# Kernel optimization log

Hardware: AMD Instinct MI355X
Metric: run time of the kernel (lower is better)

## Reference

```python
import jax, jax.numpy as jnp
import numpy as np

N = 50000      # nodes
HID = 128      # hidden_dim
E = 1600000    # edges per sparse operator (avg degree 32)


def _spmm(rows, cols, vals, x):
    # y = A @ x for COO sparse A: gather source rows, scale, scatter-add to dest rows
    return jax.ops.segment_sum(vals[:, None] * x[cols], rows, num_segments=N)


def setup_inputs() -> dict:
    key = jax.random.key(0)
    ks = jax.random.split(key, 22)

    def edges(i):
        return (jax.random.randint(ks[i], (E,), 0, N, dtype=jnp.int64) if jax.config.jax_enable_x64 else jax.random.randint(ks[i], (E,), 0, N).astype(jnp.int32),
                jax.random.randint(ks[i + 1], (E,), 0, N).astype(jnp.int32),
                jax.random.uniform(ks[i + 2], (E,), jnp.float32))

    A_rows, A_cols, A_vals = edges(0)
    P1_rows, P1_cols, P1_vals = edges(3)
    P2_rows, P2_cols, P2_vals = edges(6)
    P3_rows, P3_cols, P3_vals = edges(9)
    Ps_rows, Ps_cols, Ps_vals = edges(12)

    X = jax.random.normal(ks[15], (N, HID), jnp.float32)
    a = jax.random.normal(ks[16], (2 * HID, 1), jnp.float32) * 0.1
    W1 = jax.random.normal(ks[17], (HID, HID), jnp.float32) / jnp.sqrt(HID)
    b1 = jnp.zeros((HID,), jnp.float32)
    W2 = jax.random.normal(ks[18], (HID, HID), jnp.float32) / jnp.sqrt(HID)
    b2 = jnp.zeros((HID,), jnp.float32)

    return dict(X=X, a=a, W1=W1, b1=b1, W2=W2, b2=b2,
                A_rows=A_rows, A_cols=A_cols, A_vals=A_vals,
                P1_rows=P1_rows, P1_cols=P1_cols, P1_vals=P1_vals,
                P2_rows=P2_rows, P2_cols=P2_cols, P2_vals=P2_vals,
                P3_rows=P3_rows, P3_cols=P3_cols, P3_vals=P3_vals,
                Psct_rows=Ps_rows, Psct_cols=Ps_cols, Psct_vals=Ps_vals)


def reference(X, a, W1, b1, W2, b2,
              A_rows, A_cols, A_vals,
              P1_rows, P1_cols, P1_vals,
              P2_rows, P2_cols, P2_vals,
              P3_rows, P3_cols, P3_vals,
              Psct_rows, Psct_cols, Psct_vals):
    h = X  # [N, HID]
    h_A = _spmm(A_rows, A_cols, A_vals, h)
    h_A2 = _spmm(A_rows, A_cols, A_vals, h_A)
    h_A3 = _spmm(A_rows, A_cols, A_vals, h_A2)
    # moment = 1 => |P x| ** 1
    h_s1 = jnp.abs(_spmm(P1_rows, P1_cols, P1_vals, h))
    h_s2 = jnp.abs(_spmm(P2_rows, P2_cols, P2_vals, h))
    h_s3 = jnp.abs(_spmm(P3_rows, P3_cols, P3_vals, h))

    # Faithful to torch: cat along dim 0 then view(N, -1, 2*hid) (row-interleaved layout)
    def pair(hb):
        return jnp.concatenate([h, hb], axis=0).reshape(N, 1, 2 * HID)

    a_input = jnp.concatenate(
        [pair(h_A), pair(h_A2), pair(h_A3), pair(h_s1), pair(h_s2), pair(h_s3)],
        axis=1)  # [N, 6, 2*HID]

    e = jnp.squeeze(jax.nn.relu(a_input) @ a, axis=2)          # [N, 6]
    attention = jax.nn.softmax(e, axis=1).reshape(N, 6, 1)     # [N, 6, 1]

    # Faithful to torch: cat along dim 2 -> [N, HID, 6], then view(N, 6, -1)
    h_all = jnp.concatenate(
        [h_A[:, :, None], h_A2[:, :, None], h_A3[:, :, None],
         h_s1[:, :, None], h_s2[:, :, None], h_s3[:, :, None]],
        axis=2).reshape(N, 6, HID)

    h_prime = jnp.mean(attention * h_all, axis=1)              # [N, HID]

    # Withgres=False: skip gres smoothing (P_sct unused)
    out = jax.nn.leaky_relu(h_prime @ W1.T + b1)               # slope 0.01, matches torch default
    out = jax.nn.leaky_relu(out @ W2.T + b2)
    return out
```

## Files before the change

kernel.cpp:

```cpp
#include <hip/hip_runtime.h>
#include <hip/hip_fp16.h>

#define N_NODES 50000
#define HID 128
#define NE 1600000
#define NH (N_NODES * HID)

#define EPB   8192
#define NBLK1 196
#define NBUK  391
#define TBL   (NBUK * NBLK1)
#define SB    ((TBL + 255) / 256)
#define PTRW  (N_NODES + 2)

typedef _Float16 f16x8 __attribute__((ext_vector_type(8)));
typedef float    f32x4 __attribute__((ext_vector_type(4)));

__device__ __forceinline__ float h2f(unsigned short u) {
    __half_raw r; r.x = u;
    __half h = r;
    return __half2float(h);
}
__device__ __forceinline__ unsigned short f2h(float f) {
    __half h = __float2half_rn(f);
    __half_raw r = h;
    return r.x;
}

__global__ __launch_bounds__(256) void k1_hist4(
    const int* __restrict__ r0, const int* __restrict__ r1,
    const int* __restrict__ r2, const int* __restrict__ r3,
    int* __restrict__ table4, unsigned short* __restrict__ rank4)
{
    __shared__ int h[NBUK];
    int o = blockIdx.y, b = blockIdx.x, t = threadIdx.x;
    const int* rows = o == 0 ? r0 : o == 1 ? r1 : o == 2 ? r2 : r3;
    int* table = table4 + (size_t)o * TBL;
    unsigned short* rank = rank4 + (size_t)o * NE;

    for (int i = t; i < NBUK; i += 256) h[i] = 0;
    __syncthreads();
    int e0 = b * EPB;
    int e1 = min(e0 + EPB, NE);
    for (int e = e0 + t; e < e1; e += 256)
        rank[e] = (unsigned short)atomicAdd(&h[rows[e] >> 7], 1);
    __syncthreads();
    for (int i = t; i < NBUK; i += 256) table[i * NBLK1 + b] = h[i];
}

__global__ __launch_bounds__(256) void s1_partial4(
    const int* __restrict__ table4, int* __restrict__ part4)
{
    __shared__ int red[256];
    int o = blockIdx.y, b = blockIdx.x, t = threadIdx.x;
    const int* table = table4 + (size_t)o * TBL;
    int idx = b * 256 + t;
    red[t] = (idx < TBL) ? table[idx] : 0;
    __syncthreads();
    #pragma unroll
    for (int s = 128; s > 0; s >>= 1) {
        if (t < s) red[t] += red[t + s];
        __syncthreads();
    }
    if (t == 0) part4[o * SB + b] = red[0];
}

__global__ __launch_bounds__(1024) void s2_scan4(int* __restrict__ part4)
{
    __shared__ int sh[1024];
    int o = blockIdx.x, t = threadIdx.x;
    int* part = part4 + o * SB;
    sh[t] = (t < SB) ? part[t] : 0;
    __syncthreads();
    for (int off = 1; off < 1024; off <<= 1) {
        int v = (t >= off) ? sh[t - off] : 0;
        __syncthreads();
        sh[t] += v;
        __syncthreads();
    }
    if (t < SB) part[t] = (t == 0) ? 0 : sh[t - 1];
}

__global__ __launch_bounds__(256) void s3_add4(
    int* __restrict__ table4, const int* __restrict__ part4)
{
    __shared__ int sh[256];
    int o = blockIdx.y, b = blockIdx.x, t = threadIdx.x;
    int* table = table4 + (size_t)o * TBL;
    int idx = b * 256 + t;
    int v = (idx < TBL) ? table[idx] : 0;
    sh[t] = v;
    __syncthreads();
    #pragma unroll
    for (int off = 1; off < 256; off <<= 1) {
        int u = (t >= off) ? sh[t - off] : 0;
        __syncthreads();
        sh[t] += u;
        __syncthreads();
    }
    int excl = (t == 0) ? 0 : sh[t - 1];
    if (idx < TBL) table[idx] = part4[o * SB + b] + excl;
}

__global__ __launch_bounds__(256) void k3_scatter4(
    const int* __restrict__ r0, const int* __restrict__ r1,
    const int* __restrict__ r2, const int* __restrict__ r3,
    const int* __restrict__ c0, const int* __restrict__ c1,
    const int* __restrict__ c2, const int* __restrict__ c3,
    const float* __restrict__ v0, const float* __restrict__ v1,
    const float* __restrict__ v2, const float* __restrict__ v3,
    const unsigned short* __restrict__ rank4,
    const int* __restrict__ table4, int2* __restrict__ tmp4)
{
    __shared__ int base[NBUK];
    int o = blockIdx.y, b = blockIdx.x, t = threadIdx.x;
    const int*   rows = o == 0 ? r0 : o == 1 ? r1 : o == 2 ? r2 : r3;
    const int*   cols = o == 0 ? c0 : o == 1 ? c1 : o == 2 ? c2 : c3;
    const float* vals = o == 0 ? v0 : o == 1 ? v1 : o == 2 ? v2 : v3;
    const int* table = table4 + (size_t)o * TBL;
    const unsigned short* rank = rank4 + (size_t)o * NE;
    int2* tmp = tmp4 + (size_t)o * NE;

    for (int i = t; i < NBUK; i += 256) base[i] = table[i * NBLK1 + b];
    __syncthreads();
    int e0 = b * EPB;
    int e1 = min(e0 + EPB, NE);
    for (int e = e0 + t; e < e1; e += 256) {
        int r = rows[e];
        int pos = base[r >> 7] + (int)rank[e];
        unsigned pk = ((unsigned)cols[e] << 16) | (unsigned)f2h(vals[e]);
        tmp[pos] = make_int2(r & 127, (int)pk);
    }
}

__global__ __launch_bounds__(256) void k4_fine4(
    const int* __restrict__ table4, const int2* __restrict__ tmp4,
    unsigned* __restrict__ pairs4, int* __restrict__ ptr4)
{
    __shared__ int cnt[128];
    __shared__ int sh[256];
    __shared__ int nxt[128];
    int o = blockIdx.y, k = blockIdx.x, t = threadIdx.x;
    const int* table = table4 + (size_t)o * TBL;
    const int2* tmp = tmp4 + (size_t)o * NE;
    unsigned* pairs = pairs4 + (size_t)o * NE;
    int* rowptr = ptr4 + (size_t)o * PTRW;

    if (t < 128) cnt[t] = 0;
    __syncthreads();
    int base = table[k * NBLK1];
    int end  = (k == NBUK - 1) ? NE : table[(k + 1) * NBLK1];
    for (int e = base + t; e < end; e += 256)
        atomicAdd(&cnt[tmp[e].x], 1);
    __syncthreads();
    sh[t] = (t < 128) ? cnt[t] : 0;
    __syncthreads();
    #pragma unroll
    for (int off = 1; off < 256; off <<= 1) {
        int v = (t >= off) ? sh[t - off] : 0;
        __syncthreads();
        sh[t] += v;
        __syncthreads();
    }
    if (t < 128) {
        int excl = (t == 0) ? 0 : sh[t - 1];
        nxt[t] = base + excl;
        int row = k * 128 + t;
        if (row < N_NODES) rowptr[row] = base + excl;
    }
    if (k == NBUK - 1 && t == 255) rowptr[N_NODES] = NE;
    __syncthreads();
    for (int e = base + t; e < end; e += 256) {
        int2 p = tmp[e];
        int pos = atomicAdd(&nxt[p.x], 1);
        pairs[pos] = (unsigned)p.y;
    }
}

__global__ __launch_bounds__(256) void cvt_f2h_kernel(
    const float* __restrict__ in, unsigned short* __restrict__ out, int n4)
{
    int i = blockIdx.x * 256 + threadIdx.x;
    if (i >= n4) return;
    float4 v = ((const float4*)in)[i];
    ushort4 o;
    o.x = f2h(v.x); o.y = f2h(v.y); o.z = f2h(v.z); o.w = f2h(v.w);
    ((ushort4*)out)[i] = o;
}

__device__ __forceinline__ void spmm_row(
    const unsigned short* __restrict__ xh, const unsigned* __restrict__ pairs,
    int start, int end, int sub, bool do_abs,
    unsigned short* __restrict__ yrow)
{
    const ushort4* x4 = (const ushort4*)xh + sub;

    float4 a0 = {0,0,0,0}, a1 = {0,0,0,0};
    float4 a2 = {0,0,0,0}, a3 = {0,0,0,0};

    #define EDGE_P(P, A) { \
        unsigned _p = (P); \
        float _v = h2f((unsigned short)(_p & 0xFFFFu)); \
        ushort4 _x = x4[(size_t)(_p >> 16) * 32]; \
        A.x += _v * h2f(_x.x); \
        A.y += _v * h2f(_x.y); \
        A.z += _v * h2f(_x.z); \
        A.w += _v * h2f(_x.w); }

    int e = start;
    for (; e + 3 < end; e += 4) {
        unsigned p0 = pairs[e];
        unsigned p1 = pairs[e + 1];
        unsigned p2 = pairs[e + 2];
        unsigned p3 = pairs[e + 3];
        EDGE_P(p0, a0); EDGE_P(p1, a1); EDGE_P(p2, a2); EDGE_P(p3, a3);
    }
    for (; e < end; ++e) {
        EDGE_P(pairs[e], a0);
    }
    #undef EDGE_P

    float4 acc;
    acc.x = (a0.x + a1.x) + (a2.x + a3.x);
    acc.y = (a0.y + a1.y) + (a2.y + a3.y);
    acc.z = (a0.z + a1.z) + (a2.z + a3.z);
    acc.w = (a0.w + a1.w) + (a2.w + a3.w);
    if (do_abs) {
        acc.x = fabsf(acc.x); acc.y = fabsf(acc.y);
        acc.z = fabsf(acc.z); acc.w = fabsf(acc.w);
    }
    ushort4 o;
    o.x = f2h(acc.x); o.y = f2h(acc.y); o.z = f2h(acc.z); o.w = f2h(acc.w);
    ((ushort4*)yrow)[sub] = o;
}

__global__ __launch_bounds__(256) void spmm4_kernel(
    const int* __restrict__ ptr4, const unsigned* __restrict__ pairs4,
    const unsigned short* __restrict__ Xh, unsigned short* __restrict__ B16)
{
    int bid = blockIdx.x;
    int op  = bid & 3;
    int rb  = bid >> 2;
    int r   = rb * 8 + (threadIdx.x >> 5);
    int sub = threadIdx.x & 31;
    if (r >= N_NODES) return;

    const int*      ptr   = ptr4 + (size_t)op * PTRW;
    const unsigned* pairs = pairs4 + (size_t)op * NE;
    int dst = op ? op + 2 : 0;
    unsigned short* yrow = B16 + (size_t)dst * NH + (size_t)r * HID;

    spmm_row(Xh, pairs, ptr[r], ptr[r + 1], sub, op != 0, yrow);
}

__global__ __launch_bounds__(256) void spmm_chain_kernel(
    const int* __restrict__ ptr, const unsigned* __restrict__ pairs,
    const unsigned short* __restrict__ src16, unsigned short* __restrict__ dst16)
{
    int t   = blockIdx.x * 256 + threadIdx.x;
    int r   = t >> 5;
    int sub = t & 31;
    if (r >= N_NODES) return;
    spmm_row(src16, pairs, ptr[r], ptr[r + 1], sub, false,
             dst16 + (size_t)r * HID);
}

__global__ __launch_bounds__(256) void attn_kernel(
    const float* __restrict__ X, const unsigned short* __restrict__ B16,
    const float* __restrict__ a, float* __restrict__ att)
{
    int wid  = (blockIdx.x * 256 + threadIdx.x) >> 6;
    int lane = threadIdx.x & 63;
    if (wid >= N_NODES) return;

    const float4 av = ((const float4*)a)[lane];
    float e[6];

    if (wid < N_NODES / 2) {
        const float4 p = ((const float4*)(X + (size_t)wid * 256))[lane];
        float s = fmaxf(p.x, 0.f) * av.x + fmaxf(p.y, 0.f) * av.y +
                  fmaxf(p.z, 0.f) * av.z + fmaxf(p.w, 0.f) * av.w;
        #pragma unroll
        for (int m = 1; m < 64; m <<= 1) s += __shfl_xor(s, m);
        #pragma unroll
        for (int b = 0; b < 6; ++b) e[b] = s;
    } else {
        int m = 2 * wid - N_NODES;
        #pragma unroll
        for (int b = 0; b < 6; ++b) {
            ushort4 u = ((const ushort4*)(B16 + (size_t)b * NH +
                                          (size_t)m * HID))[lane];
            float s = fmaxf(h2f(u.x), 0.f) * av.x + fmaxf(h2f(u.y), 0.f) * av.y +
                      fmaxf(h2f(u.z), 0.f) * av.z + fmaxf(h2f(u.w), 0.f) * av.w;
            #pragma unroll
            for (int k = 1; k < 64; k <<= 1) s += __shfl_xor(s, k);
            e[b] = s;
        }
    }

    if (lane == 0) {
        float mx = e[0];
        #pragma unroll
        for (int b = 1; b < 6; ++b) mx = fmaxf(mx, e[b]);
        float ex[6], sum = 0.f;
        #pragma unroll
        for (int b = 0; b < 6; ++b) { ex[b] = expf(e[b] - mx); sum += ex[b]; }
        float inv = 1.f / sum;
        #pragma unroll
        for (int b = 0; b < 6; ++b) att[(size_t)wid * 6 + b] = ex[b] * inv;
    }
}

__global__ __launch_bounds__(256) void hprime_kernel(
    const unsigned short* __restrict__ B16, const float* __restrict__ att,
    unsigned short* __restrict__ hp16)
{
    int idx = blockIdx.x * 256 + threadIdx.x;
    if (idx >= NH) return;
    int n = idx >> 7;
    int q = idx & 127;
    float s = 0.f;
    #pragma unroll
    for (int p = 0; p < 6; ++p) {
        int f = p * HID + q;
        int j = f % 6;
        int i = f / 6;
        s += att[(size_t)n * 6 + p] *
             h2f(B16[(size_t)j * NH + (size_t)n * HID + i]);
    }
    hp16[idx] = f2h(s * (1.0f / 6.0f));
}

template <bool OUT16>
__global__ __launch_bounds__(256) void fc_mfma_kernel(
    const unsigned short* __restrict__ Ah,
    const unsigned short* __restrict__ Wh,
    const float* __restrict__ bias,
    void* __restrict__ outp)
{
    const int wid  = blockIdx.x * 4 + (threadIdx.x >> 6);
    const int lane = threadIdx.x & 63;
    const int cb   = wid & 7;
    const int o    = cb * 16 + (lane & 15);
    const int kg   = lane >> 4;
    const int nw   = (gridDim.x * 4) >> 3;

    f16x8 bfrag[4];
    #pragma unroll
    for (int ks = 0; ks < 4; ++ks)
        bfrag[ks] = *(const f16x8*)(Wh + (size_t)o * HID + ks * 32 + kg * 8);
    const float bo = bias[o];

    for (int tile = wid >> 3; tile < N_NODES / 16; tile += nw) {
        const int n0 = tile * 16;
        const unsigned short* ar =
            Ah + (size_t)(n0 + (lane & 15)) * HID + kg * 8;
        f32x4 acc = {0.f, 0.f, 0.f, 0.f};
        #pragma unroll
        for (int ks = 0; ks < 4; ++ks) {
            f16x8 af = *(const f16x8*)(ar + ks * 32);
            acc = __builtin_amdgcn_mfma_f32_16x16x32_f16(af, bfrag[ks], acc,
                                                         0, 0, 0);
        }
        #pragma unroll
        for (int j = 0; j < 4; ++j) {
            float v = acc[j] + bo;
            v = v > 0.f ? v : 0.01f * v;
            int n = n0 + kg * 4 + j;
            if (OUT16)
                ((unsigned short*)outp)[(size_t)n * HID + o] = f2h(v);
            else
                ((float*)outp)[(size_t)n * HID + o] = v;
        }
    }
}

extern "C" void kernel_launch(void* const* d_in, const int* in_sizes, int n_in,
                              void* d_out, int out_size, void* d_ws, size_t ws_size,
                              hipStream_t stream)
{
    const float* X  = (const float*)d_in[0];
    const float* a  = (const float*)d_in[1];
    const float* W1 = (const float*)d_in[2];
    const float* b1 = (const float*)d_in[3];
    const float* W2 = (const float*)d_in[4];
    const float* b2 = (const float*)d_in[5];
    const int*   op_rows[4] = { (const int*)d_in[6],  (const int*)d_in[9],
                                (const int*)d_in[12], (const int*)d_in[15] };
    const int*   op_cols[4] = { (const int*)d_in[7],  (const int*)d_in[10],
                                (const int*)d_in[13], (const int*)d_in[16] };
    const float* op_vals[4] = { (const float*)d_in[8],  (const float*)d_in[11],
                                (const float*)d_in[14], (const float*)d_in[17] };

    float* ws = (float*)d_ws;
    size_t off = 0;
    unsigned short* B16 = (unsigned short*)(ws + off);  off += (size_t)6 * NH / 2;
    float* att = ws + off;                              off += (size_t)6 * N_NODES;
    unsigned short* Xh  = (unsigned short*)(ws + off);  off += NH / 2;
    unsigned short* Wh1 = (unsigned short*)(ws + off);  off += HID * HID / 2;
    unsigned short* Wh2 = (unsigned short*)(ws + off);  off += HID * HID / 2;
    int*   ptr4   = (int*)(ws + off);                   off += (size_t)4 * PTRW;
    int*   table4 = (int*)(ws + off);                   off += (size_t)4 * TBL;
    int*   part4  = (int*)(ws + off);                   off += 4 * SB + 8;
    unsigned short* rank4 = (unsigned short*)(ws + off); off += (size_t)4 * NE / 2;
    off = (off + 3) & ~(size_t)3;
    int2*     tmp4   = (int2*)(ws + off);               off += (size_t)8 * NE;
    unsigned* pairs4 = (unsigned*)(ws + off);           off += (size_t)4 * NE;
    unsigned short* hp16  = (unsigned short*)tmp4;
    unsigned short* mid16 = (unsigned short*)pairs4;

    dim3 blk(256);
    const int rg = (N_NODES * 32 + 255) / 256;
    const int cg = (NH / 4 + 255) / 256;
    const int wg = (HID * HID / 4 + 255) / 256;

    cvt_f2h_kernel<<<cg, blk, 0, stream>>>(X, Xh, NH / 4);
    cvt_f2h_kernel<<<wg, blk, 0, stream>>>(W1, Wh1, HID * HID / 4);
    cvt_f2h_kernel<<<wg, blk, 0, stream>>>(W2, Wh2, HID * HID / 4);

    k1_hist4<<<dim3(NBLK1, 4), blk, 0, stream>>>(
        op_rows[0], op_rows[1], op_rows[2], op_rows[3], table4, rank4);
    s1_partial4<<<dim3(SB, 4), blk, 0, stream>>>(table4, part4);
    s2_scan4<<<4, 1024, 0, stream>>>(part4);
    s3_add4<<<dim3(SB, 4), blk, 0, stream>>>(table4, part4);
    k3_scatter4<<<dim3(NBLK1, 4), blk, 0, stream>>>(
        op_rows[0], op_rows[1], op_rows[2], op_rows[3],
        op_cols[0], op_cols[1], op_cols[2], op_cols[3],
        op_vals[0], op_vals[1], op_vals[2], op_vals[3],
        rank4, table4, tmp4);
    k4_fine4<<<dim3(NBUK, 4), blk, 0, stream>>>(table4, tmp4, pairs4, ptr4);

    spmm4_kernel<<<rg * 4, blk, 0, stream>>>(ptr4, pairs4, Xh, B16);

    spmm_chain_kernel<<<rg, blk, 0, stream>>>(ptr4, pairs4,
                                              B16 + 0 * (size_t)NH,
                                              B16 + 1 * (size_t)NH);
    spmm_chain_kernel<<<rg, blk, 0, stream>>>(ptr4, pairs4,
                                              B16 + 1 * (size_t)NH,
                                              B16 + 2 * (size_t)NH);

    attn_kernel<<<(N_NODES + 3) / 4, blk, 0, stream>>>(X, B16, a, att);
    hprime_kernel<<<(NH + 255) / 256, blk, 0, stream>>>(B16, att, hp16);
    fc_mfma_kernel<true ><<<1024, blk, 0, stream>>>(hp16,  Wh1, b1, mid16);
    fc_mfma_kernel<false><<<1024, blk, 0, stream>>>(mid16, Wh2, b2, d_out);
}
```

Measured before the change: 611.5 us.

## Fuse h_prime computation and both FC layers into one tiled kernel

Replaces the separate hprime kernel and two fc_mfma launches with a single tail kernel. Each block processes 128 nodes, keeping the h_prime and intermediate tiles in LDS so they never go to global memory. This removes two launches and the fp16 round trips of hp16 and mid16 through HBM. The cost is a large LDS footprint per block (about 70 KB), which lowers occupancy, and W1/W2 fragments are reloaded per block.

```diff
diff --git a/kernel.cpp b/kernel.cpp
--- a/kernel.cpp
+++ b/kernel.cpp
@@ -3,8 +3,8 @@
 
 #define N_NODES 50000
 #define HID 128
+#define NH (N_NODES * HID)
 #define NE 1600000
-#define NH (N_NODES * HID)
 
 #define EPB   8192
 #define NBLK1 196
@@ -12,6 +12,9 @@
 #define TBL   (NBUK * NBLK1)
 #define SB    ((TBL + 255) / 256)
 #define PTRW  (N_NODES + 2)
+
+#define TROWS 128
+#define TPAD  136
 
 typedef _Float16 f16x8 __attribute__((ext_vector_type(8)));
 typedef float    f32x4 __attribute__((ext_vector_type(4)));
@@ -311,66 +314,101 @@
     }
 }
 
-__global__ __launch_bounds__(256) void hprime_kernel(
+__global__ __launch_bounds__(256) void tail_kernel(
     const unsigned short* __restrict__ B16, const float* __restrict__ att,
-    unsigned short* __restrict__ hp16)
-{
-    int idx = blockIdx.x * 256 + threadIdx.x;
-    if (idx >= NH) return;
-    int n = idx >> 7;
-    int q = idx & 127;
-    float s = 0.f;
+    const unsigned short* __restrict__ Wh1, const float* __restrict__ b1,
+    const unsigned short* __restrict__ Wh2, const float* __restrict__ b2,
+    float* __restrict__ outp)
+{
+    __shared__ __align__(16) unsigned short hp[TROWS][TPAD];
+    __shared__ __align__(16) unsigned short md[TROWS][TPAD];
+    __shared__ float att_l[TROWS * 6];
+
+    const int t  = threadIdx.x;
+    const int n0 = blockIdx.x * TROWS;
+
+    for (int i = t; i < TROWS * 6; i += 256)
+        att_l[i] = att[min((size_t)n0 * 6 + i, (size_t)N_NODES * 6 - 1)];
+    __syncthreads();
+
+    #pragma unroll 2
+    for (int i = 0; i < (TROWS * HID) / 256; ++i) {
+        int idx = i * 256 + t;
+        int rl = idx >> 7, q = idx & 127;
+        int n = min(n0 + rl, N_NODES - 1);
+        float s = 0.f;
+        #pragma unroll
+        for (int p = 0; p < 6; ++p) {
+            int f = p * HID + q;
+            int j = f % 6;
+            int ii = f / 6;
+            s += att_l[rl * 6 + p] *
+                 h2f(B16[(size_t)j * NH + (size_t)n * HID + ii]);
+        }
+        hp[rl][q] = f2h(s * (1.0f / 6.0f));
+    }
+    __syncthreads();
+
+    const int lane = t & 63;
+    const int wv   = t >> 6;
+    const int lr   = lane & 15;
+    const int kg   = lane >> 4;
+
     #pragma unroll
-    for (int p = 0; p < 6; ++p) {
-        int f = p * HID + q;
-        int j = f % 6;
-        int i = f / 6;
-        s += att[(size_t)n * 6 + p] *
-             h2f(B16[(size_t)j * NH + (size_t)n * HID + i]);
-    }
-    hp16[idx] = f2h(s * (1.0f / 6.0f));
-}
-
-template <bool OUT16>
-__global__ __launch_bounds__(256) void fc_mfma_kernel(
-    const unsigned short* __restrict__ Ah,
-    const unsigned short* __restrict__ Wh,
-    const float* __restrict__ bias,
-    void* __restrict__ outp)
-{
-    const int wid  = blockIdx.x * 4 + (threadIdx.x >> 6);
-    const int lane = threadIdx.x & 63;
-    const int cb   = wid & 7;
-    const int o    = cb * 16 + (lane & 15);
-    const int kg   = lane >> 4;
-    const int nw   = (gridDim.x * 4) >> 3;
-
-    f16x8 bfrag[4];
+    for (int ci = 0; ci < 2; ++ci) {
+        int cb = wv * 2 + ci;
+        int o  = cb * 16 + lr;
+        f16x8 bf[4];
+        #pragma unroll
+        for (int ks = 0; ks < 4; ++ks)
+            bf[ks] = *(const f16x8*)(Wh1 + (size_t)o * HID + ks * 32 + kg * 8);
+        float bo = b1[o];
+        #pragma unroll
+        for (int rt = 0; rt < 8; ++rt) {
+            f32x4 acc = {0.f, 0.f, 0.f, 0.f};
+            #pragma unroll
+            for (int ks = 0; ks < 4; ++ks) {
+                f16x8 af = *(const f16x8*)&hp[rt * 16 + lr][ks * 32 + kg * 8];
+                acc = __builtin_amdgcn_mfma_f32_16x16x32_f16(af, bf[ks], acc,
+                                                             0, 0, 0);
+            }
+            #pragma unroll
+            for (int j = 0; j < 4; ++j) {
+                float v = acc[j] + bo;
+                v = v > 0.f ? v : 0.01f * v;
+                md[rt * 16 + kg * 4 + j][o] = f2h(v);
+            }
+        }
+    }
+    __syncthreads();
+
     #pragma unroll
-    for (int ks = 0; ks < 4; ++ks)
-        bfrag[ks] = *(const f16x8*)(Wh + (size_t)o * HID + ks * 32 + kg * 8);
-    const float bo = bias[o];
-
-    for (int tile = wid >> 3; tile < N_NODES / 16; tile += nw) {
-        const int n0 = tile * 16;
-        const unsigned short* ar =
-            Ah + (size_t)(n0 + (lane & 15)) * HID + kg * 8;
-        f32x4 acc = {0.f, 0.f, 0.f, 0.f};
-        #pragma unroll
-        for (int ks = 0; ks < 4; ++ks) {
-            f16x8 af = *(const f16x8*)(ar + ks * 32);
-            acc = __builtin_amdgcn_mfma_f32_16x16x32_f16(af, bfrag[ks], acc,
-                                                         0, 0, 0);
-        }
-        #pragma unroll
-        for (int j = 0; j < 4; ++j) {
-            float v = acc[j] + bo;
-            v = v > 0.f ? v : 0.01f * v;
-            int n = n0 + kg * 4 + j;
-            if (OUT16)
-                ((unsigned short*)outp)[(size_t)n * HID + o] = f2h(v);
-            else
-                ((float*)outp)[(size_t)n * HID + o] = v;
+    for (int ci = 0; ci < 2; ++ci) {
+        int cb = wv * 2 + ci;
+        int o  = cb * 16 + lr;
+        f16x8 bf[4];
+        #pragma unroll
+        for (int ks = 0; ks < 4; ++ks)
+            bf[ks] = *(const f16x8*)(Wh2 + (size_t)o * HID + ks * 32 + kg * 8);
+        float bo = b2[o];
+        #pragma unroll
+        for (int rt = 0; rt < 8; ++rt) {
+            f32x4 acc = {0.f, 0.f, 0.f, 0.f};
+            #pragma unroll
+            for (int ks = 0; ks < 4; ++ks) {
+                f16x8 af = *(const f16x8*)&md[rt * 16 + lr][ks * 32 + kg * 8];
+                acc = __builtin_amdgcn_mfma_f32_16x16x32_f16(af, bf[ks], acc,
+                                                             0, 0, 0);
+            }
+            #pragma unroll
+            for (int j = 0; j < 4; ++j) {
+                int n = n0 + rt * 16 + kg * 4 + j;
+                if (n < N_NODES) {
+                    float v = acc[j] + bo;
+                    v = v > 0.f ? v : 0.01f * v;
+                    outp[(size_t)n * HID + o] = v;
+                }
+            }
         }
     }
 }
@@ -406,13 +444,12 @@
     off = (off + 3) & ~(size_t)3;
     int2*     tmp4   = (int2*)(ws + off);               off += (size_t)8 * NE;
     unsigned* pairs4 = (unsigned*)(ws + off);           off += (size_t)4 * NE;
-    unsigned short* hp16  = (unsigned short*)tmp4;
-    unsigned short* mid16 = (unsigned short*)pairs4;
 
     dim3 blk(256);
     const int rg = (N_NODES * 32 + 255) / 256;
     const int cg = (NH / 4 + 255) / 256;
     const int wg = (HID * HID / 4 + 255) / 256;
+    const int tg = (N_NODES + TROWS - 1) / TROWS;
 
     cvt_f2h_kernel<<<cg, blk, 0, stream>>>(X, Xh, NH / 4);
     cvt_f2h_kernel<<<wg, blk, 0, stream>>>(W1, Wh1, HID * HID / 4);
@@ -440,7 +477,6 @@
                                               B16 + 2 * (size_t)NH);
 
     attn_kernel<<<(N_NODES + 3) / 4, blk, 0, stream>>>(X, B16, a, att);
-    hprime_kernel<<<(NH + 255) / 256, blk, 0, stream>>>(B16, att, hp16);
-    fc_mfma_kernel<true ><<<1024, blk, 0, stream>>>(hp16,  Wh1, b1, mid16);
-    fc_mfma_kernel<false><<<1024, blk, 0, stream>>>(mid16, Wh2, b2, d_out);
-}
+    tail_kernel<<<tg, blk, 0, stream>>>(B16, att, Wh1, b1, Wh2, b2,
+                                        (float*)d_out);
+}
```

Result: no change. 602.1 us (-1.5%).
